# Kernel optimization log

Measured on AMD Instinct MI355X. Metric: run time of the kernel, lower is better.

## Reference

```python
import jax, jax.numpy as jnp
import numpy as np

B, S, C_IN, C_OUT = 8, 2048, 512, 512

def setup_inputs() -> dict:
    key = jax.random.key(0)
    k1, k2, k3, k4 = jax.random.split(key, 4)
    sc = 1.0 / np.sqrt(C_IN)
    return {
        "x": jax.random.normal(k1, (B, S, C_IN), dtype=jnp.float32),
        "Wq": jax.random.normal(k2, (C_OUT, C_IN), dtype=jnp.float32) * sc,
        "Wk": jax.random.normal(k3, (C_OUT, C_IN), dtype=jnp.float32) * sc,
        "Wv": jax.random.normal(k4, (C_OUT, C_IN), dtype=jnp.float32) * sc,
    }

def reference(x, Wq, Wk, Wv):
    # x: [B,S,Cin]; weights [Cout,Cin] (torch Linear convention, no bias)
    C = Wq.shape[0]
    dk = jnp.sqrt(jnp.float32(1.0) / C)  # torch: sqrt(1/out_features)
    q = jnp.einsum('bsi,oi->bso', x, Wq)
    k = jnp.einsum('bsi,oi->bso', x, Wk)
    v = jnp.einsum('bsi,oi->bso', x, Wv)
    phi_q = jax.nn.elu(q * dk) + 1.0
    phi_k = jax.nn.elu(k * dk) + 1.0
    b = x.shape[0]
    mem0 = jnp.zeros((b, C, C), x.dtype)   # running sum of phi_k v^T
    zeta0 = jnp.zeros((b, C), x.dtype)     # running sum of phi_k
    def step(carry, inp):
        mem, zeta = carry
        pq, pk, vv = inp                    # each [B,C]
        dm = pk[:, :, None] * vv[:, None, :]              # [B,C,C]
        scale = jnp.einsum('bc,bc->b', pq, pk + zeta) + 1e-5
        num = jnp.einsum('bc,bcd->bd', pq, dm + mem)
        y = num / scale[:, None]
        # state updates are under torch.no_grad -> detach
        new_mem = jax.lax.stop_gradient(mem + dm)
        new_zeta = jax.lax.stop_gradient(zeta + pk)
        return (new_mem, new_zeta), y
    xs = (phi_q.transpose(1, 0, 2), phi_k.transpose(1, 0, 2), v.transpose(1, 0, 2))
    _, ys = jax.lax.scan(step, (mem0, zeta0), xs)  # ys: [S,B,C]
    return ys.transpose(1, 0, 2)                   # [B,S,C]
```

## Files before the change

kernel.cpp:

```cpp
#include <hip/hip_runtime.h>


constexpr int Bn  = 8;
constexpr int Sn  = 2048;
constexpr int Cn  = 512;
constexpr int Tn  = 128;
constexpr int NCn = 16;
constexpr float DKf = 0.04419417382415922f;

typedef __attribute__((ext_vector_type(8))) short bf16x8;
typedef __attribute__((ext_vector_type(4))) float f32x4;

__device__ __forceinline__ unsigned short f2bf(float f) {
  unsigned u = __float_as_uint(f);
  u = (u + 0x7fffu + ((u >> 16) & 1u)) >> 16;
  return (unsigned short)u;
}
__device__ __forceinline__ float bf2f(unsigned short h) {
  return __uint_as_float(((unsigned)h) << 16);
}
__device__ __forceinline__ float phi_f(float u) {
  float s = u * DKf;
  return s > 0.0f ? s + 1.0f : __expf(s);
}

__device__ __forceinline__ void stage128x32(const unsigned short* __restrict__ g,
                                            int ld, unsigned short* lds,
                                            int wid, int lane) {
#pragma unroll
  for (int cc = 0; cc < 2; ++cc) {
    const int row = cc * 64 + wid * 16 + (lane >> 2);
    const int ks  = (lane & 3) ^ ((row >> 1) & 3);
    const unsigned short* src = g + (size_t)row * ld + ks * 8;
    unsigned short* dst = lds + (size_t)(cc * 256 + wid * 64) * 8;
    __builtin_amdgcn_global_load_lds(
        (const __attribute__((address_space(1))) void*)src,
        (__attribute__((address_space(3))) void*)dst, 16, 0, 0);
  }
}

__device__ __forceinline__ void mm_loop(const unsigned short* __restrict__ Ag, int lda,
                                        const unsigned short* __restrict__ Bg, int ldb,
                                        int nkt,
                                        unsigned short* Al, unsigned short* Bl,
                                        f32x4 acc[4][4]) {
  const int t = threadIdx.x, wid = t >> 6, lane = t & 63;
  const int wm = wid >> 1, wn = wid & 1;
  const int fr = lane & 15, kb = lane >> 4;
  stage128x32(Ag, lda, Al, wid, lane);
  stage128x32(Bg, ldb, Bl, wid, lane);
  if (nkt > 1) {
    stage128x32(Ag + 32, lda, Al + 4096, wid, lane);
    stage128x32(Bg + 32, ldb, Bl + 4096, wid, lane);
  }
  int cur = 0;
  for (int kt = 0; kt < nkt; ++kt) {
    if (kt + 2 < nkt) {
      const int nx2 = (cur + 2 >= 3) ? cur - 1 : cur + 2;
      stage128x32(Ag + (kt + 2) * 32, lda, Al + nx2 * 4096, wid, lane);
      stage128x32(Bg + (kt + 2) * 32, ldb, Bl + nx2 * 4096, wid, lane);
      asm volatile("s_waitcnt vmcnt(8)" ::: "memory");
    } else if (kt + 1 < nkt) {
      asm volatile("s_waitcnt vmcnt(4)" ::: "memory");
    } else {
      asm volatile("s_waitcnt vmcnt(0)" ::: "memory");
    }
    __builtin_amdgcn_s_barrier();
    asm volatile("" ::: "memory");
    const unsigned short* Ac = Al + cur * 4096;
    const unsigned short* Bc = Bl + cur * 4096;
    bf16x8 af[4], bf[4];
#pragma unroll
    for (int m = 0; m < 4; ++m) {
      const int r = wm * 64 + m * 16 + fr;
      af[m] = *(const bf16x8*)&Ac[r * 32 + ((kb ^ ((r >> 1) & 3)) << 3)];
    }
#pragma unroll
    for (int n = 0; n < 4; ++n) {
      const int r = wn * 64 + n * 16 + fr;
      bf[n] = *(const bf16x8*)&Bc[r * 32 + ((kb ^ ((r >> 1) & 3)) << 3)];
    }
#pragma unroll
    for (int m = 0; m < 4; ++m)
#pragma unroll
      for (int n = 0; n < 4; ++n)
        acc[m][n] = __builtin_amdgcn_mfma_f32_16x16x32_bf16(af[m], bf[n], acc[m][n], 0, 0, 0);
    __builtin_amdgcn_s_barrier();
    asm volatile("" ::: "memory");
    cur = (cur + 1 >= 3) ? 0 : cur + 1;
  }
}

__global__ __launch_bounds__(256) void k_cast_x(const float* __restrict__ x,
                                                unsigned short* __restrict__ xb) {
  const size_t i8 = ((size_t)blockIdx.x * 256 + threadIdx.x) * 8;
  float4 a = *(const float4*)&x[i8];
  float4 b = *(const float4*)&x[i8 + 4];
  uint4 o;
  o.x = (unsigned)f2bf(a.x) | ((unsigned)f2bf(a.y) << 16);
  o.y = (unsigned)f2bf(a.z) | ((unsigned)f2bf(a.w) << 16);
  o.z = (unsigned)f2bf(b.x) | ((unsigned)f2bf(b.y) << 16);
  o.w = (unsigned)f2bf(b.z) | ((unsigned)f2bf(b.w) << 16);
  *(uint4*)&xb[i8] = o;
}

__global__ __launch_bounds__(256) void k_cast_w(const float* __restrict__ Wq,
                                                const float* __restrict__ Wk,
                                                const float* __restrict__ Wv,
                                                unsigned short* __restrict__ Wb) {
  const int z = blockIdx.y;
  const float* __restrict__ src = (z == 0) ? Wq : (z == 1 ? Wk : Wv);
  const size_t i8 = ((size_t)blockIdx.x * 256 + threadIdx.x) * 8;
  float4 a = *(const float4*)&src[i8];
  float4 b = *(const float4*)&src[i8 + 4];
  uint4 o;
  o.x = (unsigned)f2bf(a.x) | ((unsigned)f2bf(a.y) << 16);
  o.y = (unsigned)f2bf(a.z) | ((unsigned)f2bf(a.w) << 16);
  o.z = (unsigned)f2bf(b.x) | ((unsigned)f2bf(b.y) << 16);
  o.w = (unsigned)f2bf(b.z) | ((unsigned)f2bf(b.w) << 16);
  *(uint4*)&Wb[(size_t)z * Cn * Cn + i8] = o;
}

__global__ __launch_bounds__(256) void k_proj(
    const unsigned short* __restrict__ xb, const unsigned short* __restrict__ Wb,
    unsigned short* __restrict__ PQ, unsigned short* __restrict__ PK,
    unsigned short* __restrict__ PKt, unsigned short* __restrict__ Vt,
    float* __restrict__ zsum)
{
  __shared__ unsigned short Al[3 * 128 * 32], Bl[3 * 128 * 32];
  __shared__ float zbuf[2][128];
  const int bid = blockIdx.x;
  const int xcd = bid & 7, idx = bid >> 3;
  const int n = idx & 3, z = (idx >> 2) % 3, mloc = idx / 12;
  const int n0 = n * 128, m0 = (xcd * 16 + mloc) * 128;
  const int t = threadIdx.x, wid = t >> 6, lane = t & 63;
  const int wm = wid >> 1, wn = wid & 1;
  f32x4 acc[4][4];
  const f32x4 zero = {0.f, 0.f, 0.f, 0.f};
#pragma unroll
  for (int m = 0; m < 4; ++m)
#pragma unroll
    for (int nn = 0; nn < 4; ++nn) acc[m][nn] = zero;

  mm_loop(xb + (size_t)m0 * Cn, Cn,
          Wb + (size_t)z * Cn * Cn + (size_t)n0 * Cn, Cn, Cn / 32, Al, Bl, acc);

  float ps[4] = {0.f, 0.f, 0.f, 0.f};
#pragma unroll
  for (int m = 0; m < 4; ++m)
#pragma unroll
    for (int nn = 0; nn < 4; ++nn) {
      const int row0 = m0 + wm * 64 + m * 16 + ((lane >> 4) << 2);
      const int col  = n0 + wn * 64 + nn * 16 + (lane & 15);
      f32x4 v = acc[m][nn];
      if (z == 0) {
#pragma unroll
        for (int j = 0; j < 4; ++j)
          PQ[(size_t)(row0 + j) * Cn + col] = f2bf(phi_f(v[j]));
      } else if (z == 1) {
        ushort4 p;
#pragma unroll
        for (int j = 0; j < 4; ++j) {
          unsigned short u = f2bf(phi_f(v[j]));
          PK[(size_t)(row0 + j) * Cn + col] = u;
          (&p.x)[j] = u;
          ps[nn] += bf2f(u);
        }
        const int b = row0 >> 11, tq = row0 & (Sn - 1);
        *(ushort4*)&PKt[((size_t)b * Cn + col) * Sn + tq] = p;
      } else {
        ushort4 p;
#pragma unroll
        for (int j = 0; j < 4; ++j) (&p.x)[j] = f2bf(v[j]);
        const int b = row0 >> 11, tq = row0 & (Sn - 1);
        *(ushort4*)&Vt[((size_t)b * Cn + col) * Sn + tq] = p;
      }
    }

  if (z == 1) {
#pragma unroll
    for (int nn = 0; nn < 4; ++nn) {
      float v = ps[nn];
      v += __shfl_xor(v, 16); v += __shfl_xor(v, 32);
      if (lane < 16) zbuf[wm][wn * 64 + nn * 16 + lane] = v;
    }
    __syncthreads();
    if (t < 128) {
      const int b = m0 >> 11, ch = (m0 >> 7) & 15;
      zsum[((size_t)b * NCn + ch) * Cn + n0 + t] = zbuf[0][t] + zbuf[1][t];
    }
  }
}

__global__ __launch_bounds__(256) void k_gram(
    const unsigned short* __restrict__ PQ, const unsigned short* __restrict__ PK,
    const float* __restrict__ zsum,
    unsigned short* __restrict__ Abuf, float* __restrict__ scale)
{
  __shared__ unsigned short Al[3 * 128 * 32], Bl[3 * 128 * 32];
  __shared__ float rsmem[2][128];
  __shared__ float zpl[512];
  const int b = blockIdx.y, ch = blockIdx.x;
  const size_t base = ((size_t)b * Sn + ch * Tn) * Cn;
  f32x4 acc[4][4];
  const f32x4 zero = {0.f, 0.f, 0.f, 0.f};
#pragma unroll
  for (int m = 0; m < 4; ++m)
#pragma unroll
    for (int n = 0; n < 4; ++n) acc[m][n] = zero;

  mm_loop(PQ + base, Cn, PK + base, Cn, Cn / 32, Al, Bl, acc);

  const int t = threadIdx.x, wid = t >> 6, lane = t & 63;
  const int wm = wid >> 1, wn = wid & 1;
  float rsum[4][4];
#pragma unroll
  for (int m = 0; m < 4; ++m)
#pragma unroll
    for (int j = 0; j < 4; ++j) rsum[m][j] = 0.f;
#pragma unroll
  for (int m = 0; m < 4; ++m)
#pragma unroll
    for (int n = 0; n < 4; ++n) {
      f32x4 v = acc[m][n];
#pragma unroll
      for (int j = 0; j < 4; ++j) {
        const int row = wm * 64 + m * 16 + ((lane >> 4) << 2) + j;
        const int col = wn * 64 + n * 16 + (lane & 15);
        unsigned short u = (col <= row) ? f2bf(v[j]) : 0;
        Abuf[((size_t)(b * NCn + ch) * Tn + row) * Tn + col] = u;
        rsum[m][j] += bf2f(u);
      }
    }
#pragma unroll
  for (int m = 0; m < 4; ++m)
#pragma unroll
    for (int j = 0; j < 4; ++j) {
      float r = rsum[m][j];
      r += __shfl_xor(r, 1); r += __shfl_xor(r, 2);
      r += __shfl_xor(r, 4); r += __shfl_xor(r, 8);
      if ((lane & 15) == 0)
        rsmem[wn][wm * 64 + m * 16 + ((lane >> 4) << 2) + j] = r;
    }
#pragma unroll
  for (int e = 0; e < 2; ++e) {
    const int c = t + e * 256;
    float s = 0.f;
    for (int ch2 = 0; ch2 < ch; ++ch2)
      s += zsum[((size_t)b * NCn + ch2) * Cn + c];
    zpl[c] = s;
  }
  __syncthreads();
  const int row = t >> 1, half = (t & 1) * 256;
  const unsigned short* pq = PQ + base + (size_t)row * Cn + half;
  float dacc = 0.f;
  for (int i = 0; i < 256; i += 8) {
    uint4 q = *(const uint4*)(pq + i);
    dacc += bf2f((unsigned short)(q.x & 0xffff)) * zpl[half + i + 0]
          + bf2f((unsigned short)(q.x >> 16))    * zpl[half + i + 1]
          + bf2f((unsigned short)(q.y & 0xffff)) * zpl[half + i + 2]
          + bf2f((unsigned short)(q.y >> 16))    * zpl[half + i + 3]
          + bf2f((unsigned short)(q.z & 0xffff)) * zpl[half + i + 4]
          + bf2f((unsigned short)(q.z >> 16))    * zpl[half + i + 5]
          + bf2f((unsigned short)(q.w & 0xffff)) * zpl[half + i + 6]
          + bf2f((unsigned short)(q.w >> 16))    * zpl[half + i + 7];
  }
  dacc += __shfl_xor(dacc, 1);
  if ((t & 1) == 0)
    scale[(size_t)b * Sn + ch * Tn + row] =
        rsmem[0][row] + rsmem[1][row] + dacc + 1e-5f;
}

__device__ __forceinline__ void stage64x128(const unsigned short* __restrict__ g,
                                            int ld, unsigned short* lds,
                                            int wid, int lane) {
#pragma unroll
  for (int i = 0; i < 4; ++i) {
    const int row = wid * 16 + i * 4 + (lane >> 4);
    const int s   = (lane & 15) ^ (row & 7);
    const unsigned short* src = g + (size_t)row * ld + s * 8;
    unsigned short* dst = lds + (size_t)(wid * 16 + i * 4) * 128;
    __builtin_amdgcn_global_load_lds(
        (const __attribute__((address_space(1))) void*)src,
        (__attribute__((address_space(3))) void*)dst, 16, 0, 0);
  }
}

__global__ __launch_bounds__(256) void k_kvp(
    const unsigned short* __restrict__ PKt, const unsigned short* __restrict__ Vt,
    unsigned short* __restrict__ Mpre)
{
  __shared__ unsigned short Al[2 * 64 * 128], Bl[2 * 64 * 128];
  const int bid = blockIdx.x;
  const int b = bid & 7, idx = bid >> 3;
  const int d0 = (idx & 7) * 64, c0 = (idx >> 3) * 64;
  const int t = threadIdx.x, wid = t >> 6, lane = t & 63;
  const int wm = wid >> 1, wn = wid & 1;
  const int fr = lane & 15, kb = lane >> 4;
  f32x4 acc[2][2];
  const f32x4 zero = {0.f, 0.f, 0.f, 0.f};
#pragma unroll
  for (int m = 0; m < 2; ++m)
#pragma unroll
    for (int n = 0; n < 2; ++n) acc[m][n] = zero;
  const unsigned short* Ag = PKt + ((size_t)b * Cn + c0) * Sn;
  const unsigned short* Bg = Vt  + ((size_t)b * Cn + d0) * Sn;
  stage64x128(Ag, Sn, Al, wid, lane);
  stage64x128(Bg, Sn, Bl, wid, lane);
  int cur = 0;
  for (int ch = 0; ch < NCn; ++ch) {
    const int nxt = cur ^ 1;
    if (ch + 1 < NCn) {
      stage64x128(Ag + (ch + 1) * Tn, Sn, Al + nxt * 8192, wid, lane);
      stage64x128(Bg + (ch + 1) * Tn, Sn, Bl + nxt * 8192, wid, lane);
      asm volatile("s_waitcnt vmcnt(8)" ::: "memory");
    } else {
      asm volatile("s_waitcnt vmcnt(0)" ::: "memory");
    }
    __builtin_amdgcn_s_barrier();
    asm volatile("" ::: "memory");
    if (ch > 0) {
#pragma unroll
      for (int m = 0; m < 2; ++m)
#pragma unroll
        for (int n = 0; n < 2; ++n) {
          const int c_row = c0 + wm * 32 + m * 16 + (kb << 2);
          const int d     = d0 + wn * 32 + n * 16 + fr;
          ushort4 p;
#pragma unroll
          for (int j = 0; j < 4; ++j) (&p.x)[j] = f2bf(acc[m][n][j]);
          *(ushort4*)&Mpre[((size_t)(b * NCn + ch) * Cn + d) * Cn + c_row] = p;
        }
    }
    const unsigned short* Ac = Al + cur * 8192;
    const unsigned short* Bc = Bl + cur * 8192;
#pragma unroll
    for (int kt = 0; kt < 4; ++kt) {
      bf16x8 af[2], bf[2];
#pragma unroll
      for (int m = 0; m < 2; ++m) {
        const int r = wm * 32 + m * 16 + fr;
        af[m] = *(const bf16x8*)&Ac[r * 128 + (((kt * 4 + kb) ^ (r & 7)) << 3)];
      }
#pragma unroll
      for (int n = 0; n < 2; ++n) {
        const int r = wn * 32 + n * 16 + fr;
        bf[n] = *(const bf16x8*)&Bc[r * 128 + (((kt * 4 + kb) ^ (r & 7)) << 3)];
      }
#pragma unroll
      for (int m = 0; m < 2; ++m)
#pragma unroll
        for (int n = 0; n < 2; ++n)
          acc[m][n] = __builtin_amdgcn_mfma_f32_16x16x32_bf16(af[m], bf[n], acc[m][n], 0, 0, 0);
    }
    __builtin_amdgcn_s_barrier();
    asm volatile("" ::: "memory");
    cur = nxt;
  }
}

__global__ __launch_bounds__(256) void k_avinter(
    const unsigned short* __restrict__ Abuf, const unsigned short* __restrict__ Vt,
    const unsigned short* __restrict__ PQ, const unsigned short* __restrict__ Mpre,
    const float* __restrict__ scale, float* __restrict__ out)
{
  __shared__ unsigned short Al[3 * 128 * 32], Bl[3 * 128 * 32];
  const int bid = blockIdx.x;
  const int logical = (bid & 7) * 64 + (bid >> 3);
  const int d0 = (logical & 3) * 128;
  const int ch = (logical >> 2) & 15;
  const int b  = logical >> 6;
  const int t0 = ch * Tn;
  f32x4 acc[4][4];
  const f32x4 zero = {0.f, 0.f, 0.f, 0.f};
#pragma unroll
  for (int m = 0; m < 4; ++m)
#pragma unroll
    for (int n = 0; n < 4; ++n) acc[m][n] = zero;

  mm_loop(Abuf + (size_t)(b * NCn + ch) * Tn * Tn, Tn,
          Vt + ((size_t)b * Cn + d0) * Sn + t0, Sn, Tn / 32, Al, Bl, acc);
  if (ch > 0)
    mm_loop(PQ + ((size_t)b * Sn + t0) * Cn, Cn,
            Mpre + ((size_t)(b * NCn + ch) * Cn + d0) * Cn, Cn, Cn / 32, Al, Bl, acc);

  const int t = threadIdx.x, wid = t >> 6, lane = t & 63;
  const int wm = wid >> 1, wn = wid & 1;
#pragma unroll
  for (int m = 0; m < 4; ++m)
#pragma unroll
    for (int n = 0; n < 4; ++n) {
      const int row0 = t0 + wm * 64 + m * 16 + ((lane >> 4) << 2);
      const int col  = d0 + wn * 64 + n * 16 + (lane & 15);
      f32x4 v = acc[m][n];
#pragma unroll
      for (int j = 0; j < 4; ++j) {
        const size_t sidx = (size_t)b * Sn + row0 + j;
        out[sidx * Cn + col] = v[j] / scale[sidx];
      }
    }
}

extern "C" void kernel_launch(void* const* d_in, const int* in_sizes, int n_in,
                              void* d_out, int out_size, void* d_ws, size_t ws_size,
                              hipStream_t stream)
{
  const float* x  = (const float*)d_in[0];
  const float* Wq = (const float*)d_in[1];
  const float* Wk = (const float*)d_in[2];
  const float* Wv = (const float*)d_in[3];
  float* out = (float*)d_out;

  unsigned short* xb   = (unsigned short*)d_ws;
  unsigned short* Wb   = xb   + (size_t)Bn * Sn * Cn;
  unsigned short* PQ   = Wb   + (size_t)3 * Cn * Cn;
  unsigned short* PK   = PQ   + (size_t)Bn * Sn * Cn;
  unsigned short* PKt  = PK   + (size_t)Bn * Sn * Cn;
  unsigned short* Vt   = PKt  + (size_t)Bn * Sn * Cn;
  unsigned short* Abuf = Vt   + (size_t)Bn * Sn * Cn;
  unsigned short* Mpre = Abuf + (size_t)Bn * NCn * Tn * Tn;
  float* scale = (float*)(Mpre + (size_t)Bn * NCn * Cn * Cn);
  float* zsum  = scale + (size_t)Bn * Sn;
  (void)ws_size; (void)in_sizes; (void)n_in; (void)out_size;

  hipLaunchKernelGGL(k_cast_x, dim3(4096), dim3(256), 0, stream, x, xb);
  hipLaunchKernelGGL(k_cast_w, dim3(128, 3), dim3(256), 0, stream, Wq, Wk, Wv, Wb);
  hipLaunchKernelGGL(k_proj, dim3(1536), dim3(256), 0, stream, xb, Wb, PQ, PK, PKt, Vt, zsum);
  hipLaunchKernelGGL(k_gram, dim3(NCn, Bn), dim3(256), 0, stream, PQ, PK, zsum, Abuf, scale);
  hipLaunchKernelGGL(k_kvp, dim3(512), dim3(256), 0, stream, PKt, Vt, Mpre);
  hipLaunchKernelGGL(k_avinter, dim3(512), dim3(256), 0, stream, Abuf, Vt, PQ, Mpre, scale, out);
}
```

Baseline: 132.2 us.

## Split gram kernel across row halves, fuse cast launches, pipeline avinter k-loops

Merges the x and weight cast kernels into one launch to drop a launch. Splits the gram kernel into two 64-row blocks per chunk, doubling the grid from 128 blocks so more CUs stay busy. Merges the intra- and inter-chunk matmuls in k_avinter into one continuous triple-buffered k loop, avoiding a pipeline drain between them. Adds s_setprio around the MFMA sections to favour the math waves, which may change scheduling in unexpected ways.

```diff
diff --git a/kernel.cpp b/kernel.cpp
--- a/kernel.cpp
+++ b/kernel.cpp
@@ -80,37 +80,38 @@
       const int r = wn * 64 + n * 16 + fr;
       bf[n] = *(const bf16x8*)&Bc[r * 32 + ((kb ^ ((r >> 1) & 3)) << 3)];
     }
+    __builtin_amdgcn_s_setprio(1);
 #pragma unroll
     for (int m = 0; m < 4; ++m)
 #pragma unroll
       for (int n = 0; n < 4; ++n)
         acc[m][n] = __builtin_amdgcn_mfma_f32_16x16x32_bf16(af[m], bf[n], acc[m][n], 0, 0, 0);
+    __builtin_amdgcn_s_setprio(0);
     __builtin_amdgcn_s_barrier();
     asm volatile("" ::: "memory");
     cur = (cur + 1 >= 3) ? 0 : cur + 1;
   }
 }
 
-__global__ __launch_bounds__(256) void k_cast_x(const float* __restrict__ x,
-                                                unsigned short* __restrict__ xb) {
-  const size_t i8 = ((size_t)blockIdx.x * 256 + threadIdx.x) * 8;
-  float4 a = *(const float4*)&x[i8];
-  float4 b = *(const float4*)&x[i8 + 4];
-  uint4 o;
-  o.x = (unsigned)f2bf(a.x) | ((unsigned)f2bf(a.y) << 16);
-  o.y = (unsigned)f2bf(a.z) | ((unsigned)f2bf(a.w) << 16);
-  o.z = (unsigned)f2bf(b.x) | ((unsigned)f2bf(b.y) << 16);
-  o.w = (unsigned)f2bf(b.z) | ((unsigned)f2bf(b.w) << 16);
-  *(uint4*)&xb[i8] = o;
-}
-
-__global__ __launch_bounds__(256) void k_cast_w(const float* __restrict__ Wq,
-                                                const float* __restrict__ Wk,
-                                                const float* __restrict__ Wv,
-                                                unsigned short* __restrict__ Wb) {
-  const int z = blockIdx.y;
-  const float* __restrict__ src = (z == 0) ? Wq : (z == 1 ? Wk : Wv);
-  const size_t i8 = ((size_t)blockIdx.x * 256 + threadIdx.x) * 8;
+__global__ __launch_bounds__(256) void k_cast(
+    const float* __restrict__ x, const float* __restrict__ Wq,
+    const float* __restrict__ Wk, const float* __restrict__ Wv,
+    unsigned short* __restrict__ xb, unsigned short* __restrict__ Wb)
+{
+  const int bid = blockIdx.x;
+  const float* src;
+  unsigned short* dst;
+  size_t i8;
+  if (bid < 4096) {
+    i8 = ((size_t)bid * 256 + threadIdx.x) * 8;
+    src = x; dst = xb;
+  } else {
+    const size_t f = ((size_t)(bid - 4096) * 256 + threadIdx.x) * 8;
+    const int z = (int)(f >> 18);
+    src = (z == 0) ? Wq : (z == 1 ? Wk : Wv);
+    dst = Wb + ((size_t)z << 18);
+    i8 = f & ((1u << 18) - 1);
+  }
   float4 a = *(const float4*)&src[i8];
   float4 b = *(const float4*)&src[i8 + 4];
   uint4 o;
@@ -118,7 +119,7 @@
   o.y = (unsigned)f2bf(a.z) | ((unsigned)f2bf(a.w) << 16);
   o.z = (unsigned)f2bf(b.x) | ((unsigned)f2bf(b.y) << 16);
   o.w = (unsigned)f2bf(b.z) | ((unsigned)f2bf(b.w) << 16);
-  *(uint4*)&Wb[(size_t)z * Cn * Cn + i8] = o;
+  *(uint4*)&dst[i8] = o;
 }
 
 __global__ __launch_bounds__(256) void k_proj(
@@ -192,27 +193,90 @@
   }
 }
 
+__device__ __forceinline__ void stageA64(const unsigned short* __restrict__ g,
+                                         unsigned short* lds, int wid, int lane) {
+  const int row = wid * 16 + (lane >> 2);
+  const int ks  = (lane & 3) ^ ((row >> 1) & 3);
+  __builtin_amdgcn_global_load_lds(
+      (const __attribute__((address_space(1))) void*)(g + (size_t)row * Cn + ks * 8),
+      (__attribute__((address_space(3))) void*)(lds + wid * 512), 16, 0, 0);
+}
+__device__ __forceinline__ void stageB128(const unsigned short* __restrict__ g,
+                                          unsigned short* lds, int wid, int lane) {
+#pragma unroll
+  for (int e = 0; e < 2; ++e) {
+    const int row = e * 64 + wid * 16 + (lane >> 2);
+    const int ks  = (lane & 3) ^ ((row >> 1) & 3);
+    __builtin_amdgcn_global_load_lds(
+        (const __attribute__((address_space(1))) void*)(g + (size_t)row * Cn + ks * 8),
+        (__attribute__((address_space(3))) void*)(lds + e * 2048 + wid * 512),
+        16, 0, 0);
+  }
+}
+
 __global__ __launch_bounds__(256) void k_gram(
     const unsigned short* __restrict__ PQ, const unsigned short* __restrict__ PK,
     const float* __restrict__ zsum,
     unsigned short* __restrict__ Abuf, float* __restrict__ scale)
 {
-  __shared__ unsigned short Al[3 * 128 * 32], Bl[3 * 128 * 32];
-  __shared__ float rsmem[2][128];
+  __shared__ unsigned short Asl[3 * 2048], Bsl[3 * 4096];
+  __shared__ float rsmem[4][64];
   __shared__ float zpl[512];
-  const int b = blockIdx.y, ch = blockIdx.x;
-  const size_t base = ((size_t)b * Sn + ch * Tn) * Cn;
-  f32x4 acc[4][4];
+  const int b = blockIdx.z, ch = blockIdx.y, i0 = blockIdx.x * 64;
+  const unsigned short* Aq = PQ + ((size_t)(b * Sn + ch * Tn + i0)) * Cn;
+  const unsigned short* Bk = PK + ((size_t)(b * Sn + ch * Tn)) * Cn;
+  const int t = threadIdx.x, wid = t >> 6, lane = t & 63;
+  const int fr = lane & 15, kb = lane >> 4;
+  f32x4 acc[4][2];
   const f32x4 zero = {0.f, 0.f, 0.f, 0.f};
 #pragma unroll
   for (int m = 0; m < 4; ++m)
 #pragma unroll
-    for (int n = 0; n < 4; ++n) acc[m][n] = zero;
-
-  mm_loop(PQ + base, Cn, PK + base, Cn, Cn / 32, Al, Bl, acc);
-
-  const int t = threadIdx.x, wid = t >> 6, lane = t & 63;
-  const int wm = wid >> 1, wn = wid & 1;
+    for (int n = 0; n < 2; ++n) acc[m][n] = zero;
+
+  stageA64(Aq, Asl, wid, lane);
+  stageB128(Bk, Bsl, wid, lane);
+  stageA64(Aq + 32, Asl + 2048, wid, lane);
+  stageB128(Bk + 32, Bsl + 4096, wid, lane);
+  int cur = 0;
+  for (int kt = 0; kt < 16; ++kt) {
+    if (kt + 2 < 16) {
+      const int nx2 = (cur + 2 >= 3) ? cur - 1 : cur + 2;
+      stageA64(Aq + (kt + 2) * 32, Asl + nx2 * 2048, wid, lane);
+      stageB128(Bk + (kt + 2) * 32, Bsl + nx2 * 4096, wid, lane);
+      asm volatile("s_waitcnt vmcnt(6)" ::: "memory");
+    } else if (kt + 1 < 16) {
+      asm volatile("s_waitcnt vmcnt(3)" ::: "memory");
+    } else {
+      asm volatile("s_waitcnt vmcnt(0)" ::: "memory");
+    }
+    __builtin_amdgcn_s_barrier();
+    asm volatile("" ::: "memory");
+    const unsigned short* Ac = Asl + cur * 2048;
+    const unsigned short* Bc = Bsl + cur * 4096;
+    bf16x8 af[4], bf[2];
+#pragma unroll
+    for (int m = 0; m < 4; ++m) {
+      const int r = m * 16 + fr;
+      af[m] = *(const bf16x8*)&Ac[r * 32 + ((kb ^ ((r >> 1) & 3)) << 3)];
+    }
+#pragma unroll
+    for (int n = 0; n < 2; ++n) {
+      const int c = wid * 32 + n * 16 + fr;
+      bf[n] = *(const bf16x8*)&Bc[c * 32 + ((kb ^ ((c >> 1) & 3)) << 3)];
+    }
+    __builtin_amdgcn_s_setprio(1);
+#pragma unroll
+    for (int m = 0; m < 4; ++m)
+#pragma unroll
+      for (int n = 0; n < 2; ++n)
+        acc[m][n] = __builtin_amdgcn_mfma_f32_16x16x32_bf16(af[m], bf[n], acc[m][n], 0, 0, 0);
+    __builtin_amdgcn_s_setprio(0);
+    __builtin_amdgcn_s_barrier();
+    asm volatile("" ::: "memory");
+    cur = (cur + 1 >= 3) ? 0 : cur + 1;
+  }
+
   float rsum[4][4];
 #pragma unroll
   for (int m = 0; m < 4; ++m)
@@ -221,14 +285,14 @@
 #pragma unroll
   for (int m = 0; m < 4; ++m)
 #pragma unroll
-    for (int n = 0; n < 4; ++n) {
+    for (int n = 0; n < 2; ++n) {
       f32x4 v = acc[m][n];
 #pragma unroll
       for (int j = 0; j < 4; ++j) {
-        const int row = wm * 64 + m * 16 + ((lane >> 4) << 2) + j;
-        const int col = wn * 64 + n * 16 + (lane & 15);
-        unsigned short u = (col <= row) ? f2bf(v[j]) : 0;
-        Abuf[((size_t)(b * NCn + ch) * Tn + row) * Tn + col] = u;
+        const int row_g = i0 + m * 16 + kb * 4 + j;
+        const int col   = wid * 32 + n * 16 + fr;
+        unsigned short u = (col <= row_g) ? f2bf(v[j]) : 0;
+        Abuf[((size_t)(b * NCn + ch) * Tn + row_g) * Tn + col] = u;
         rsum[m][j] += bf2f(u);
       }
     }
@@ -239,8 +303,7 @@
       float r = rsum[m][j];
       r += __shfl_xor(r, 1); r += __shfl_xor(r, 2);
       r += __shfl_xor(r, 4); r += __shfl_xor(r, 8);
-      if ((lane & 15) == 0)
-        rsmem[wn][wm * 64 + m * 16 + ((lane >> 4) << 2) + j] = r;
+      if (fr == 0) rsmem[wid][m * 16 + kb * 4 + j] = r;
     }
 #pragma unroll
   for (int e = 0; e < 2; ++e) {
@@ -251,24 +314,25 @@
     zpl[c] = s;
   }
   __syncthreads();
-  const int row = t >> 1, half = (t & 1) * 256;
-  const unsigned short* pq = PQ + base + (size_t)row * Cn + half;
+  const int row = t >> 2, q4 = (t & 3) * 128;
+  const unsigned short* pq = Aq + (size_t)row * Cn + q4;
   float dacc = 0.f;
-  for (int i = 0; i < 256; i += 8) {
+  for (int i = 0; i < 128; i += 8) {
     uint4 q = *(const uint4*)(pq + i);
-    dacc += bf2f((unsigned short)(q.x & 0xffff)) * zpl[half + i + 0]
-          + bf2f((unsigned short)(q.x >> 16))    * zpl[half + i + 1]
-          + bf2f((unsigned short)(q.y & 0xffff)) * zpl[half + i + 2]
-          + bf2f((unsigned short)(q.y >> 16))    * zpl[half + i + 3]
-          + bf2f((unsigned short)(q.z & 0xffff)) * zpl[half + i + 4]
-          + bf2f((unsigned short)(q.z >> 16))    * zpl[half + i + 5]
-          + bf2f((unsigned short)(q.w & 0xffff)) * zpl[half + i + 6]
-          + bf2f((unsigned short)(q.w >> 16))    * zpl[half + i + 7];
+    dacc += bf2f((unsigned short)(q.x & 0xffff)) * zpl[q4 + i + 0]
+          + bf2f((unsigned short)(q.x >> 16))    * zpl[q4 + i + 1]
+          + bf2f((unsigned short)(q.y & 0xffff)) * zpl[q4 + i + 2]
+          + bf2f((unsigned short)(q.y >> 16))    * zpl[q4 + i + 3]
+          + bf2f((unsigned short)(q.z & 0xffff)) * zpl[q4 + i + 4]
+          + bf2f((unsigned short)(q.z >> 16))    * zpl[q4 + i + 5]
+          + bf2f((unsigned short)(q.w & 0xffff)) * zpl[q4 + i + 6]
+          + bf2f((unsigned short)(q.w >> 16))    * zpl[q4 + i + 7];
   }
   dacc += __shfl_xor(dacc, 1);
-  if ((t & 1) == 0)
-    scale[(size_t)b * Sn + ch * Tn + row] =
-        rsmem[0][row] + rsmem[1][row] + dacc + 1e-5f;
+  dacc += __shfl_xor(dacc, 2);
+  if ((t & 3) == 0)
+    scale[(size_t)b * Sn + ch * Tn + i0 + row] =
+        rsmem[0][row] + rsmem[1][row] + rsmem[2][row] + rsmem[3][row] + dacc + 1e-5f;
 }
 
 __device__ __forceinline__ void stage64x128(const unsigned short* __restrict__ g,
@@ -334,6 +398,7 @@
     }
     const unsigned short* Ac = Al + cur * 8192;
     const unsigned short* Bc = Bl + cur * 8192;
+    __builtin_amdgcn_s_setprio(1);
 #pragma unroll
     for (int kt = 0; kt < 4; ++kt) {
       bf16x8 af[2], bf[2];
@@ -353,6 +418,7 @@
         for (int n = 0; n < 2; ++n)
           acc[m][n] = __builtin_amdgcn_mfma_f32_16x16x32_bf16(af[m], bf[n], acc[m][n], 0, 0, 0);
     }
+    __builtin_amdgcn_s_setprio(0);
     __builtin_amdgcn_s_barrier();
     asm volatile("" ::: "memory");
     cur = nxt;
@@ -371,6 +437,9 @@
   const int ch = (logical >> 2) & 15;
   const int b  = logical >> 6;
   const int t0 = ch * Tn;
+  const int t = threadIdx.x, wid = t >> 6, lane = t & 63;
+  const int wm = wid >> 1, wn = wid & 1;
+  const int fr = lane & 15, kb = lane >> 4;
   f32x4 acc[4][4];
   const f32x4 zero = {0.f, 0.f, 0.f, 0.f};
 #pragma unroll
@@ -378,14 +447,59 @@
 #pragma unroll
     for (int n = 0; n < 4; ++n) acc[m][n] = zero;
 
-  mm_loop(Abuf + (size_t)(b * NCn + ch) * Tn * Tn, Tn,
-          Vt + ((size_t)b * Cn + d0) * Sn + t0, Sn, Tn / 32, Al, Bl, acc);
-  if (ch > 0)
-    mm_loop(PQ + ((size_t)b * Sn + t0) * Cn, Cn,
-            Mpre + ((size_t)(b * NCn + ch) * Cn + d0) * Cn, Cn, Cn / 32, Al, Bl, acc);
-
-  const int t = threadIdx.x, wid = t >> 6, lane = t & 63;
-  const int wm = wid >> 1, wn = wid & 1;
+  const unsigned short* Aintra = Abuf + (size_t)(b * NCn + ch) * Tn * Tn;
+  const unsigned short* Bintra = Vt + ((size_t)b * Cn + d0) * Sn + t0;
+  const unsigned short* Ainter = PQ + ((size_t)b * Sn + t0) * Cn;
+  const unsigned short* Binter = Mpre + ((size_t)(b * NCn + ch) * Cn + d0) * Cn;
+  auto srcA = [&](int kt) { return (kt < 4) ? Aintra + kt * 32 : Ainter + (kt - 4) * 32; };
+  auto srcB = [&](int kt) { return (kt < 4) ? Bintra + kt * 32 : Binter + (kt - 4) * 32; };
+  auto ldA  = [&](int kt) { return (kt < 4) ? Tn : Cn; };
+  auto ldB  = [&](int kt) { return (kt < 4) ? Sn : Cn; };
+  const int nkt = (ch > 0) ? 20 : 4;
+
+  stage128x32(srcA(0), ldA(0), Al, wid, lane);
+  stage128x32(srcB(0), ldB(0), Bl, wid, lane);
+  stage128x32(srcA(1), ldA(1), Al + 4096, wid, lane);
+  stage128x32(srcB(1), ldB(1), Bl + 4096, wid, lane);
+  int cur = 0;
+  for (int kt = 0; kt < nkt; ++kt) {
+    if (kt + 2 < nkt) {
+      const int nx2 = (cur + 2 >= 3) ? cur - 1 : cur + 2;
+      stage128x32(srcA(kt + 2), ldA(kt + 2), Al + nx2 * 4096, wid, lane);
+      stage128x32(srcB(kt + 2), ldB(kt + 2), Bl + nx2 * 4096, wid, lane);
+      asm volatile("s_waitcnt vmcnt(8)" ::: "memory");
+    } else if (kt + 1 < nkt) {
+      asm volatile("s_waitcnt vmcnt(4)" ::: "memory");
+    } else {
+      asm volatile("s_waitcnt vmcnt(0)" ::: "memory");
+    }
+    __builtin_amdgcn_s_barrier();
+    asm volatile("" ::: "memory");
+    const unsigned short* Ac = Al + cur * 4096;
+    const unsigned short* Bc = Bl + cur * 4096;
+    bf16x8 af[4], bf[4];
+#pragma unroll
+    for (int m = 0; m < 4; ++m) {
+      const int r = wm * 64 + m * 16 + fr;
+      af[m] = *(const bf16x8*)&Ac[r * 32 + ((kb ^ ((r >> 1) & 3)) << 3)];
+    }
+#pragma unroll
+    for (int n = 0; n < 4; ++n) {
+      const int r = wn * 64 + n * 16 + fr;
+      bf[n] = *(const bf16x8*)&Bc[r * 32 + ((kb ^ ((r >> 1) & 3)) << 3)];
+    }
+    __builtin_amdgcn_s_setprio(1);
+#pragma unroll
+    for (int m = 0; m < 4; ++m)
+#pragma unroll
+      for (int n = 0; n < 4; ++n)
+        acc[m][n] = __builtin_amdgcn_mfma_f32_16x16x32_bf16(af[m], bf[n], acc[m][n], 0, 0, 0);
+    __builtin_amdgcn_s_setprio(0);
+    __builtin_amdgcn_s_barrier();
+    asm volatile("" ::: "memory");
+    cur = (cur + 1 >= 3) ? 0 : cur + 1;
+  }
+
 #pragma unroll
   for (int m = 0; m < 4; ++m)
 #pragma unroll
@@ -423,10 +537,9 @@
   float* zsum  = scale + (size_t)Bn * Sn;
   (void)ws_size; (void)in_sizes; (void)n_in; (void)out_size;
 
-  hipLaunchKernelGGL(k_cast_x, dim3(4096), dim3(256), 0, stream, x, xb);
-  hipLaunchKernelGGL(k_cast_w, dim3(128, 3), dim3(256), 0, stream, Wq, Wk, Wv, Wb);
+  hipLaunchKernelGGL(k_cast, dim3(4096 + 384), dim3(256), 0, stream, x, Wq, Wk, Wv, xb, Wb);
   hipLaunchKernelGGL(k_proj, dim3(1536), dim3(256), 0, stream, xb, Wb, PQ, PK, PKt, Vt, zsum);
-  hipLaunchKernelGGL(k_gram, dim3(NCn, Bn), dim3(256), 0, stream, PQ, PK, zsum, Abuf, scale);
+  hipLaunchKernelGGL(k_gram, dim3(2, NCn, Bn), dim3(256), 0, stream, PQ, PK, zsum, Abuf, scale);
   hipLaunchKernelGGL(k_kvp, dim3(512), dim3(256), 0, stream, PKt, Vt, Mpre);
   hipLaunchKernelGGL(k_avinter, dim3(512), dim3(256), 0, stream, Abuf, Vt, PQ, Mpre, scale, out);
 }
```

Result: faster. 125.1 us (-5.4%).
